# Kernel tuning notes

Hardware: AMD Instinct MI355X
Metric: run time of the kernel (lower is better)

Reference implementation:

```python
import jax, jax.numpy as jnp
import numpy as np

C = 256
CQ = max(1, C // 8)  # 32


def setup_inputs() -> dict:
    key = jax.random.key(0)
    ks = jax.random.split(key, 8)
    B, D, H, W = 4, 16, 16, 16
    x = jax.random.normal(ks[0], (B, C, D, H, W), dtype=jnp.float32)
    # 1x1 Conv3d == channel-wise linear; weights scaled ~1/sqrt(C) for stable softmax
    s = 0.05
    wq = jax.random.normal(ks[1], (CQ, C), dtype=jnp.float32) * s
    bq = jax.random.normal(ks[2], (CQ,), dtype=jnp.float32) * s
    wk = jax.random.normal(ks[3], (CQ, C), dtype=jnp.float32) * s
    bk = jax.random.normal(ks[4], (CQ,), dtype=jnp.float32) * s
    wv = jax.random.normal(ks[5], (C, C), dtype=jnp.float32) * s
    bv = jax.random.normal(ks[6], (C,), dtype=jnp.float32) * s
    gamma = jax.random.normal(ks[7], (1,), dtype=jnp.float32)
    return {"x": x, "wq": wq, "bq": bq, "wk": wk, "bk": bk,
            "wv": wv, "bv": bv, "gamma": gamma}


def reference(x, wq, bq, wk, bk, wv, bv, gamma):
    B, Cc, D, H, W = x.shape
    N = D * H * W
    xf = x.reshape(B, Cc, N)                                   # [B,C,N]
    # 1x1 conv projections (channel contractions)
    q = jnp.einsum('qc,bcn->bnq', wq, xf) + bq                 # [B,N,Cq]
    k = jnp.einsum('qc,bcn->bqn', wk, xf) + bk[None, :, None]  # [B,Cq,N]
    v = jnp.einsum('oc,bcn->bon', wv, xf) + bv[None, :, None]  # [B,C,N]
    att = jax.nn.softmax(jnp.einsum('bnq,bqm->bnm', q, k), axis=-1)  # [B,N,N]
    out = jnp.einsum('bom,bnm->bon', v, att)                   # [B,C,N]
    out = gamma[0] * out + xf
    return out.reshape(B, Cc, D, H, W)
```

## Files before the change

kernel.cpp:

```cpp
#include <hip/hip_runtime.h>
#include <stdint.h>

typedef unsigned short u16;
typedef unsigned int u32;
typedef short s16x8 __attribute__((ext_vector_type(8)));
typedef float f32x4 __attribute__((ext_vector_type(4)));
typedef float f32x16 __attribute__((ext_vector_type(16)));

#define LOG2E 1.44269504088896340736f
#define FIXMAX 40.0f

__device__ __forceinline__ u16 f2bf(float f) {
    union { float f; u32 i; } c; c.f = f;
    u32 u = c.i + 0x7FFFu + ((c.i >> 16) & 1u);
    return (u16)(u >> 16);
}
__device__ __forceinline__ float fast_exp2(float x) {
#if __has_builtin(__builtin_amdgcn_exp2f)
    return __builtin_amdgcn_exp2f(x);
#else
    return exp2f(x);
#endif
}
__device__ __forceinline__ u32 cvtpk_bf16(float lo, float hi) {
    u32 r;
    asm("v_cvt_pk_bf16_f32 %0, %1, %2" : "=v"(r) : "v"(lo), "v"(hi));
    return r;
}
__device__ __forceinline__ void swap32(u32 a, u32 b, u32& x, u32& y, int half) {
#if __has_builtin(__builtin_amdgcn_permlane32_swap)
    auto r = __builtin_amdgcn_permlane32_swap(a, b, false, false);
    x = r[0]; y = r[1];
#else
    u32 ax = (u32)__shfl_xor((int)a, 32, 64);
    u32 bx = (u32)__shfl_xor((int)b, 32, 64);
    x = half ? bx : a;
    y = half ? b : ax;
#endif
}


__global__ __launch_bounds__(256) void convert_w(
    const float* __restrict__ wq, const float* __restrict__ wk,
    const float* __restrict__ wv, u16* __restrict__ wsb)
{
    int i = blockIdx.x * 256 + threadIdx.x;
    float v;
    if (i < 65536)      v = wv[i];
    else if (i < 73728) v = wq[i - 65536];
    else                v = wk[i - 73728];
    wsb[i] = f2bf(v);
}

__global__ __launch_bounds__(256, 2) void proj_kernel(
    const float* __restrict__ x,
    const u16* __restrict__ wq_bf, const float* __restrict__ bq,
    const u16* __restrict__ wk_bf, const float* __restrict__ bk,
    const u16* __restrict__ wv_bf, const float* __restrict__ bv,
    u16* __restrict__ q_ws, u16* __restrict__ k_ws, u16* __restrict__ v_ws)
{
    __shared__ u16 XT[32 * 264];
    const int t  = threadIdx.x;
    const int b  = blockIdx.x >> 7;
    const int n0 = (blockIdx.x & 127) << 5;

    {
        const int c2 = t & 127;
        const int nh = (t >> 7) << 4;
        size_t base0 = (size_t)(b * 256 + 2 * c2) * 4096 + n0 + nh;
        float4 R0[4], R1[4];
        #pragma unroll
        for (int g = 0; g < 4; ++g) {
            R0[g] = *(const float4*)(x + base0 + 4 * g);
            R1[g] = *(const float4*)(x + base0 + 4096 + 4 * g);
        }
        u32* lds32 = (u32*)XT;
        #pragma unroll
        for (int g = 0; g < 4; ++g) {
            const float* p0 = (const float*)&R0[g];
            const float* p1 = (const float*)&R1[g];
            #pragma unroll
            for (int e = 0; e < 4; ++e) {
                int nl = nh + g * 4 + e;
                lds32[nl * 132 + c2] = (u32)f2bf(p0[e]) | ((u32)f2bf(p1[e]) << 16);
            }
        }
    }
    __syncthreads();

    const int wave = t >> 6, lane = t & 63, quad = lane >> 4, l15 = lane & 15;
    const int orow = wave * 64;

    f32x4 accV[4][2];
    f32x4 accQK[2];
    #pragma unroll
    for (int i = 0; i < 4; ++i) { accV[i][0] = (f32x4)0.0f; accV[i][1] = (f32x4)0.0f; }
    accQK[0] = (f32x4)0.0f; accQK[1] = (f32x4)0.0f;

    const int qsel = wave >> 1;
    const u16* wsel = qsel ? wk_bf : wq_bf;
    const int qc = ((wave & 1) << 4) + l15;

    #pragma unroll
    for (int co = 0; co < 8; ++co) {
        int cb = co * 32 + quad * 8;
        s16x8 X0 = *(const s16x8*)(XT + l15 * 264 + cb);
        s16x8 X1 = *(const s16x8*)(XT + (16 + l15) * 264 + cb);
        s16x8 WV[4];
        #pragma unroll
        for (int rt = 0; rt < 4; ++rt)
            WV[rt] = *(const s16x8*)(wv_bf + (size_t)(orow + rt * 16 + l15) * 256 + cb);
        s16x8 WQK = *(const s16x8*)(wsel + (size_t)qc * 256 + cb);

        #pragma unroll
        for (int rt = 0; rt < 4; ++rt) {
            accV[rt][0] = __builtin_amdgcn_mfma_f32_16x16x32_bf16(WV[rt], X0, accV[rt][0], 0, 0, 0);
            accV[rt][1] = __builtin_amdgcn_mfma_f32_16x16x32_bf16(WV[rt], X1, accV[rt][1], 0, 0, 0);
        }
        accQK[0] = __builtin_amdgcn_mfma_f32_16x16x32_bf16(X0, WQK, accQK[0], 0, 0, 0);
        accQK[1] = __builtin_amdgcn_mfma_f32_16x16x32_bf16(X1, WQK, accQK[1], 0, 0, 0);
    }

    {
        const int mh = (l15 >> 3) & 1;
        const int j  = l15 & 7;
        #pragma unroll
        for (int rt = 0; rt < 4; ++rt) {
            int ob = orow + rt * 16 + quad * 4;
            float bvf[4];
            #pragma unroll
            for (int r = 0; r < 4; ++r) bvf[r] = bv[ob + r];
            #pragma unroll
            for (int ct = 0; ct < 2; ++ct) {
                int kt = ((n0 + ct * 16) >> 4);
                #pragma unroll
                for (int r = 0; r < 4; ++r) {
                    int o = ob + r;
                    size_t addr = ((((size_t)(b * 256 + kt) * 8) + (o >> 5)) << 9)
                                + (size_t)((mh << 5) + (o & 31)) * 8 + j;
                    v_ws[addr] = f2bf(accV[rt][ct][r] + bvf[r]);
                }
            }
        }
    }
    if (qsel == 0) {
        float bias = bq[qc];
        #pragma unroll
        for (int r = 0; r < 2; ++r)
            #pragma unroll
            for (int reg = 0; reg < 4; ++reg) {
                int n = n0 + r * 16 + quad * 4 + reg;
                q_ws[(size_t)(b * 4096 + n) * 32 + qc] = f2bf((accQK[r][reg] + bias) * LOG2E);
            }
    } else {
        float bias = bk[qc];
        const int ckt = qc >> 4, ch2 = (qc >> 3) & 1, cj = qc & 7;
        #pragma unroll
        for (int r = 0; r < 2; ++r)
            #pragma unroll
            for (int reg = 0; reg < 4; ++reg) {
                int m = n0 + r * 16 + quad * 4 + reg;
                size_t addr = ((((size_t)(b * 128 + (m >> 5)) * 2) + ckt) << 9)
                            + (size_t)((ch2 << 5) + (m & 31)) * 8 + cj;
                k_ws[addr] = f2bf(accQK[r][reg] + bias);
            }
    }
}

__global__ __launch_bounds__(512, 2) void attn_kernel(
    const u16* __restrict__ q_ws, const u16* __restrict__ k_ws, const u16* __restrict__ v_ws,
    const float* __restrict__ x, const float* __restrict__ gamma_p, float* __restrict__ out)
{
    __shared__ float Ored[256 * 64];
    __shared__ float l_sh[4][2][64];

    const int t = threadIdx.x;
    const int wave = t >> 6, lane = t & 63;
    const int og = wave >> 2;
    const int ms = wave & 3;
    const int half = lane >> 5, n31 = lane & 31;

    const int bid = blockIdx.x;
    const int xcd = bid & 7;
    const int b   = xcd >> 1;
    const int nt  = ((xcd & 1) << 5) | (bid >> 3);
    const int n0  = nt << 6;

    const u16* qrow0 = q_ws + ((size_t)(b * 4096 + n0 + n31) << 5) + half * 8;
    const s16x8 QA0 = *(const s16x8*)(qrow0);
    const s16x8 QA1 = *(const s16x8*)(qrow0 + 16);
    const s16x8 QB0 = *(const s16x8*)(qrow0 + 1024);
    const s16x8 QB1 = *(const s16x8*)(qrow0 + 1024 + 16);

    const u16* kfb = k_ws + (((size_t)b * 256) << 9);
    const u16* vfb = v_ws + ((size_t)b << 20);

    f32x16 accO[4][2];
    #pragma unroll
    for (int ot = 0; ot < 4; ++ot) { accO[ot][0] = (f32x16)0.0f; accO[ot][1] = (f32x16)0.0f; }
    float l0_acc = 0.0f, l1_acc = 0.0f;

    for (int ch = 0; ch < 32; ++ch) {
        const int mt  = (ms << 5) + ch;
        const int ktb = mt << 1;

        const u16* kp = kfb + ((size_t)mt << 10) + lane * 8;
        s16x8 KF0 = *(const s16x8*)(kp);
        s16x8 KF1 = *(const s16x8*)(kp + 512);

        const u16* vp = vfb + (((size_t)(ktb * 8 + og * 4)) << 9) + lane * 8;
        s16x8 V0[4], V1[4];
        #pragma unroll
        for (int ot = 0; ot < 4; ++ot) {
            V0[ot] = *(const s16x8*)(vp + ot * 512);
            V1[ot] = *(const s16x8*)(vp + 4096 + ot * 512);
        }

        f32x16 st0 = (f32x16)0.0f, st1 = (f32x16)0.0f;
        st0 = __builtin_amdgcn_mfma_f32_32x32x16_bf16(KF0, QA0, st0, 0, 0, 0);
        st0 = __builtin_amdgcn_mfma_f32_32x32x16_bf16(KF1, QA1, st0, 0, 0, 0);
        st1 = __builtin_amdgcn_mfma_f32_32x32x16_bf16(KF0, QB0, st1, 0, 0, 0);
        st1 = __builtin_amdgcn_mfma_f32_32x32x16_bf16(KF1, QB1, st1, 0, 0, 0);

        float p0[16], p1[16];
        #pragma unroll
        for (int r = 0; r < 16; ++r) p0[r] = fast_exp2(st0[r] - FIXMAX);
        #pragma unroll
        for (int r = 0; r < 16; ++r) p1[r] = fast_exp2(st1[r] - FIXMAX);
        if (og == 0) {
            float a0 = (p0[0] + p0[1]) + (p0[2] + p0[3]);
            float a1 = (p0[4] + p0[5]) + (p0[6] + p0[7]);
            float a2 = (p0[8] + p0[9]) + (p0[10] + p0[11]);
            float a3 = (p0[12] + p0[13]) + (p0[14] + p0[15]);
            l0_acc += (a0 + a1) + (a2 + a3);
            float b0 = (p1[0] + p1[1]) + (p1[2] + p1[3]);
            float b1 = (p1[4] + p1[5]) + (p1[6] + p1[7]);
            float b2 = (p1[8] + p1[9]) + (p1[10] + p1[11]);
            float b3 = (p1[12] + p1[13]) + (p1[14] + p1[15]);
            l1_acc += (b0 + b1) + (b2 + b3);
        }

        union { u32 w[4]; s16x8 v; } P0B0, P0B1, P1B0, P1B1;
        {
            u32 A0 = cvtpk_bf16(p0[0],  p0[1]),  A1 = cvtpk_bf16(p0[2],  p0[3]);
            u32 B0 = cvtpk_bf16(p0[4],  p0[5]),  B1 = cvtpk_bf16(p0[6],  p0[7]);
            u32 C0 = cvtpk_bf16(p0[8],  p0[9]),  C1 = cvtpk_bf16(p0[10], p0[11]);
            u32 D0 = cvtpk_bf16(p0[12], p0[13]), D1 = cvtpk_bf16(p0[14], p0[15]);
            u32 w0, w1, w2, w3, y0, y1, y2, y3;
            swap32(A0, B0, w0, w2, half);
            swap32(A1, B1, w1, w3, half);
            swap32(C0, D0, y0, y2, half);
            swap32(C1, D1, y1, y3, half);
            P0B0.w[0] = w0; P0B0.w[1] = w1; P0B0.w[2] = w2; P0B0.w[3] = w3;
            P0B1.w[0] = y0; P0B1.w[1] = y1; P0B1.w[2] = y2; P0B1.w[3] = y3;
        }
        {
            u32 A0 = cvtpk_bf16(p1[0],  p1[1]),  A1 = cvtpk_bf16(p1[2],  p1[3]);
            u32 B0 = cvtpk_bf16(p1[4],  p1[5]),  B1 = cvtpk_bf16(p1[6],  p1[7]);
            u32 C0 = cvtpk_bf16(p1[8],  p1[9]),  C1 = cvtpk_bf16(p1[10], p1[11]);
            u32 D0 = cvtpk_bf16(p1[12], p1[13]), D1 = cvtpk_bf16(p1[14], p1[15]);
            u32 w0, w1, w2, w3, y0, y1, y2, y3;
            swap32(A0, B0, w0, w2, half);
            swap32(A1, B1, w1, w3, half);
            swap32(C0, D0, y0, y2, half);
            swap32(C1, D1, y1, y3, half);
            P1B0.w[0] = w0; P1B0.w[1] = w1; P1B0.w[2] = w2; P1B0.w[3] = w3;
            P1B1.w[0] = y0; P1B1.w[1] = y1; P1B1.w[2] = y2; P1B1.w[3] = y3;
        }

        #pragma unroll
        for (int ot = 0; ot < 4; ++ot) {
            accO[ot][0] = __builtin_amdgcn_mfma_f32_32x32x16_bf16(V0[ot], P0B0.v, accO[ot][0], 0, 0, 0);
            accO[ot][0] = __builtin_amdgcn_mfma_f32_32x32x16_bf16(V1[ot], P0B1.v, accO[ot][0], 0, 0, 0);
            accO[ot][1] = __builtin_amdgcn_mfma_f32_32x32x16_bf16(V0[ot], P1B0.v, accO[ot][1], 0, 0, 0);
            accO[ot][1] = __builtin_amdgcn_mfma_f32_32x32x16_bf16(V1[ot], P1B1.v, accO[ot][1], 0, 0, 0);
        }
    }

    if (og == 0) {
        l_sh[ms][half][n31]      = l0_acc;
        l_sh[ms][half][32 + n31] = l1_acc;
    }
    if (ms == 0) {
        #pragma unroll
        for (int ot = 0; ot < 4; ++ot)
            #pragma unroll
            for (int nhh = 0; nhh < 2; ++nhh)
                #pragma unroll
                for (int r = 0; r < 16; ++r) {
                    const int o = (og << 7) + (ot << 5) + (r & 3) + ((r >> 2) << 3) + (half << 2);
                    Ored[(o << 6) + (nhh << 5) + n31] = accO[ot][nhh][r];
                }
    }
    __syncthreads();
    #pragma unroll
    for (int s = 1; s < 4; ++s) {
        if (ms == s) {
            #pragma unroll
            for (int ot = 0; ot < 4; ++ot)
                #pragma unroll
                for (int nhh = 0; nhh < 2; ++nhh)
                    #pragma unroll
                    for (int r = 0; r < 16; ++r) {
                        const int o = (og << 7) + (ot << 5) + (r & 3) + ((r >> 2) << 3) + (half << 2);
                        Ored[(o << 6) + (nhh << 5) + n31] += accO[ot][nhh][r];
                    }
        }
        __syncthreads();
    }

    const float gamma = gamma_p[0];
    const int nn = t & 63;
    const int oo = t >> 6;
    float lt = 0.0f;
    #pragma unroll
    for (int s = 0; s < 4; ++s) lt += l_sh[s][0][nn] + l_sh[s][1][nn];
    const float rinv = gamma / lt;
    const int n = n0 + nn;
    #pragma unroll
    for (int i = 0; i < 32; ++i) {
        const int o = oo + (i << 3);
        const size_t idx = ((size_t)(b * 256 + o) << 12) + n;
        out[idx] = Ored[(o << 6) + nn] * rinv + x[idx];
    }
}

extern "C" void kernel_launch(void* const* d_in, const int* in_sizes, int n_in,
                              void* d_out, int out_size, void* d_ws, size_t ws_size,
                              hipStream_t stream) {
    const float* x  = (const float*)d_in[0];
    const float* wq = (const float*)d_in[1];
    const float* bq = (const float*)d_in[2];
    const float* wk = (const float*)d_in[3];
    const float* bk = (const float*)d_in[4];
    const float* wv = (const float*)d_in[5];
    const float* bv = (const float*)d_in[6];
    const float* gm = (const float*)d_in[7];

    u16* wsb   = (u16*)d_ws;
    u16* wv_bf = wsb;
    u16* wq_bf = wsb + 65536;
    u16* wk_bf = wsb + 73728;
    u16* q_ws  = wsb + 81920;
    u16* k_ws  = q_ws + 4 * 4096 * 32;
    u16* v_ws  = k_ws + 4 * 4096 * 32;

    convert_w<<<320, 256, 0, stream>>>(wq, wk, wv, wsb);
    proj_kernel<<<512, 256, 0, stream>>>(x, wq_bf, bq, wk_bf, bk, wv_bf, bv, q_ws, k_ws, v_ws);
    attn_kernel<<<256, 512, 0, stream>>>(q_ws, k_ws, v_ws, x, gm, (float*)d_out);
}
```

Baseline: 145.9 us.

## Fuse weight bf16 conversion into projection kernel and prefetch K fragments

Removes the separate convert_w launch. The projection kernel now reads fp32 weights and converts them to bf16 in registers with packed cvt instructions, which saves a launch and a workspace round trip. In exchange, each block reads twice as many weight bytes and does redundant conversions. The attention loop also software-prefetches the next K fragment after the QK MFMAs, so that load latency overlaps the softmax and PV work at some register cost.

```diff
diff --git a/kernel.cpp b/kernel.cpp
--- a/kernel.cpp
+++ b/kernel.cpp
@@ -26,6 +26,16 @@
     u32 r;
     asm("v_cvt_pk_bf16_f32 %0, %1, %2" : "=v"(r) : "v"(lo), "v"(hi));
     return r;
+}
+__device__ __forceinline__ s16x8 cvt8(const float* p) {
+    float4 a = *(const float4*)(p);
+    float4 b = *(const float4*)(p + 4);
+    union { u32 w[4]; s16x8 v; } r;
+    r.w[0] = cvtpk_bf16(a.x, a.y);
+    r.w[1] = cvtpk_bf16(a.z, a.w);
+    r.w[2] = cvtpk_bf16(b.x, b.y);
+    r.w[3] = cvtpk_bf16(b.z, b.w);
+    return r.v;
 }
 __device__ __forceinline__ void swap32(u32 a, u32 b, u32& x, u32& y, int half) {
 #if __has_builtin(__builtin_amdgcn_permlane32_swap)
@@ -40,23 +50,11 @@
 }
 
 
-__global__ __launch_bounds__(256) void convert_w(
-    const float* __restrict__ wq, const float* __restrict__ wk,
-    const float* __restrict__ wv, u16* __restrict__ wsb)
-{
-    int i = blockIdx.x * 256 + threadIdx.x;
-    float v;
-    if (i < 65536)      v = wv[i];
-    else if (i < 73728) v = wq[i - 65536];
-    else                v = wk[i - 73728];
-    wsb[i] = f2bf(v);
-}
-
 __global__ __launch_bounds__(256, 2) void proj_kernel(
     const float* __restrict__ x,
-    const u16* __restrict__ wq_bf, const float* __restrict__ bq,
-    const u16* __restrict__ wk_bf, const float* __restrict__ bk,
-    const u16* __restrict__ wv_bf, const float* __restrict__ bv,
+    const float* __restrict__ wq, const float* __restrict__ bq,
+    const float* __restrict__ wk, const float* __restrict__ bk,
+    const float* __restrict__ wv, const float* __restrict__ bv,
     u16* __restrict__ q_ws, u16* __restrict__ k_ws, u16* __restrict__ v_ws)
 {
     __shared__ u16 XT[32 * 264];
@@ -98,7 +96,7 @@
     accQK[0] = (f32x4)0.0f; accQK[1] = (f32x4)0.0f;
 
     const int qsel = wave >> 1;
-    const u16* wsel = qsel ? wk_bf : wq_bf;
+    const float* wsel = qsel ? wk : wq;
     const int qc = ((wave & 1) << 4) + l15;
 
     #pragma unroll
@@ -109,8 +107,8 @@
         s16x8 WV[4];
         #pragma unroll
         for (int rt = 0; rt < 4; ++rt)
-            WV[rt] = *(const s16x8*)(wv_bf + (size_t)(orow + rt * 16 + l15) * 256 + cb);
-        s16x8 WQK = *(const s16x8*)(wsel + (size_t)qc * 256 + cb);
+            WV[rt] = cvt8(wv + (size_t)(orow + rt * 16 + l15) * 256 + cb);
+        s16x8 WQK = cvt8(wsel + (size_t)qc * 256 + cb);
 
         #pragma unroll
         for (int rt = 0; rt < 4; ++rt) {
@@ -200,13 +198,16 @@
     for (int ot = 0; ot < 4; ++ot) { accO[ot][0] = (f32x16)0.0f; accO[ot][1] = (f32x16)0.0f; }
     float l0_acc = 0.0f, l1_acc = 0.0f;
 
+    {
+        const u16* kp0 = kfb + (((size_t)(ms << 5)) << 10) + lane * 8;
+    }
+    const u16* kp0 = kfb + (((size_t)(ms << 5)) << 10) + lane * 8;
+    s16x8 KF0 = *(const s16x8*)(kp0);
+    s16x8 KF1 = *(const s16x8*)(kp0 + 512);
+
     for (int ch = 0; ch < 32; ++ch) {
         const int mt  = (ms << 5) + ch;
         const int ktb = mt << 1;
-
-        const u16* kp = kfb + ((size_t)mt << 10) + lane * 8;
-        s16x8 KF0 = *(const s16x8*)(kp);
-        s16x8 KF1 = *(const s16x8*)(kp + 512);
 
         const u16* vp = vfb + (((size_t)(ktb * 8 + og * 4)) << 9) + lane * 8;
         s16x8 V0[4], V1[4];
@@ -221,6 +222,13 @@
         st0 = __builtin_amdgcn_mfma_f32_32x32x16_bf16(KF1, QA1, st0, 0, 0, 0);
         st1 = __builtin_amdgcn_mfma_f32_32x32x16_bf16(KF0, QB0, st1, 0, 0, 0);
         st1 = __builtin_amdgcn_mfma_f32_32x32x16_bf16(KF1, QB1, st1, 0, 0, 0);
+
+        {
+            const int mtn = (ch < 31) ? mt + 1 : mt;
+            const u16* kpn = kfb + ((size_t)mtn << 10) + lane * 8;
+            KF0 = *(const s16x8*)(kpn);
+            KF1 = *(const s16x8*)(kpn + 512);
+        }
 
         float p0[16], p1[16];
         #pragma unroll
@@ -337,15 +345,10 @@
     const float* bv = (const float*)d_in[6];
     const float* gm = (const float*)d_in[7];
 
-    u16* wsb   = (u16*)d_ws;
-    u16* wv_bf = wsb;
-    u16* wq_bf = wsb + 65536;
-    u16* wk_bf = wsb + 73728;
-    u16* q_ws  = wsb + 81920;
-    u16* k_ws  = q_ws + 4 * 4096 * 32;
-    u16* v_ws  = k_ws + 4 * 4096 * 32;
-
-    convert_w<<<320, 256, 0, stream>>>(wq, wk, wv, wsb);
-    proj_kernel<<<512, 256, 0, stream>>>(x, wq_bf, bq, wk_bf, bk, wv_bf, bv, q_ws, k_ws, v_ws);
+    u16* q_ws = (u16*)d_ws;
+    u16* k_ws = q_ws + 4 * 4096 * 32;
+    u16* v_ws = k_ws + 4 * 4096 * 32;
+
+    proj_kernel<<<512, 256, 0, stream>>>(x, wq, bq, wk, bk, wv, bv, q_ws, k_ws, v_ws);
     attn_kernel<<<256, 512, 0, stream>>>(q_ws, k_ws, v_ws, x, gm, (float*)d_out);
 }
```

Measured after the change: 153.7 us. 1.05x slower.

## Software-pipeline attention loop: overlap next QK^T/softmax with current PV MFMAs

Applied to the files above, without the earlier changes.

Restructures the attention chunk loop so the S=KQ MFMAs and exp/bf16 packing for chunk i+1 are issued alongside the PV MFMAs for chunk i, with K fragments prefetched two chunks ahead. A prologue and epilogue handle the first score tile and the last PV update. The aim is to hide the exp/convert/permlane latency and the dependent MFMA chain behind independent matrix work. In exchange it carries an extra set of packed P registers, which raises register pressure and could lower occupancy under launch_bounds(256,2).

```diff
diff --git a/kernel.cpp b/kernel.cpp
--- a/kernel.cpp
+++ b/kernel.cpp
@@ -37,6 +37,33 @@
     x = half ? bx : a;
     y = half ? b : ax;
 #endif
+}
+
+union PBu { u32 w[4]; s16x8 v; };
+
+__device__ __forceinline__ void sm_half(const f32x16& st, PBu& PB0, PBu& PB1,
+                                        float& l_acc, bool doL, int half) {
+    float p[16];
+    #pragma unroll
+    for (int r = 0; r < 16; ++r) p[r] = fast_exp2(st[r] - FIXMAX);
+    if (doL) {
+        float t0 = (p[0] + p[1]) + (p[2] + p[3]);
+        float t1 = (p[4] + p[5]) + (p[6] + p[7]);
+        float t2 = (p[8] + p[9]) + (p[10] + p[11]);
+        float t3 = (p[12] + p[13]) + (p[14] + p[15]);
+        l_acc += (t0 + t1) + (t2 + t3);
+    }
+    u32 A0 = cvtpk_bf16(p[0],  p[1]),  A1 = cvtpk_bf16(p[2],  p[3]);
+    u32 B0 = cvtpk_bf16(p[4],  p[5]),  B1 = cvtpk_bf16(p[6],  p[7]);
+    u32 C0 = cvtpk_bf16(p[8],  p[9]),  C1 = cvtpk_bf16(p[10], p[11]);
+    u32 D0 = cvtpk_bf16(p[12], p[13]), D1 = cvtpk_bf16(p[14], p[15]);
+    u32 w0, w1, w2, w3, y0, y1, y2, y3;
+    swap32(A0, B0, w0, w2, half);
+    swap32(A1, B1, w1, w3, half);
+    swap32(C0, D0, y0, y2, half);
+    swap32(C1, D1, y1, y3, half);
+    PB0.w[0] = w0; PB0.w[1] = w1; PB0.w[2] = w2; PB0.w[3] = w3;
+    PB1.w[0] = y0; PB1.w[1] = y1; PB1.w[2] = y2; PB1.w[3] = y3;
 }
 
 
@@ -199,81 +226,82 @@
     #pragma unroll
     for (int ot = 0; ot < 4; ++ot) { accO[ot][0] = (f32x16)0.0f; accO[ot][1] = (f32x16)0.0f; }
     float l0_acc = 0.0f, l1_acc = 0.0f;
-
-    for (int ch = 0; ch < 32; ++ch) {
-        const int mt  = (ms << 5) + ch;
-        const int ktb = mt << 1;
-
-        const u16* kp = kfb + ((size_t)mt << 10) + lane * 8;
-        s16x8 KF0 = *(const s16x8*)(kp);
-        s16x8 KF1 = *(const s16x8*)(kp + 512);
-
-        const u16* vp = vfb + (((size_t)(ktb * 8 + og * 4)) << 9) + lane * 8;
-        s16x8 V0[4], V1[4];
-        #pragma unroll
-        for (int ot = 0; ot < 4; ++ot) {
-            V0[ot] = *(const s16x8*)(vp + ot * 512);
-            V1[ot] = *(const s16x8*)(vp + 4096 + ot * 512);
-        }
-
+    const bool doL = (og == 0);
+
+    const int mtb = ms << 5;
+
+    s16x8 KF0, KF1;
+    {
+        const u16* kp = kfb + ((size_t)mtb << 10) + lane * 8;
+        KF0 = *(const s16x8*)(kp);
+        KF1 = *(const s16x8*)(kp + 512);
+    }
+    PBu pA0, pA1, pB0, pB1;
+    {
         f32x16 st0 = (f32x16)0.0f, st1 = (f32x16)0.0f;
         st0 = __builtin_amdgcn_mfma_f32_32x32x16_bf16(KF0, QA0, st0, 0, 0, 0);
         st0 = __builtin_amdgcn_mfma_f32_32x32x16_bf16(KF1, QA1, st0, 0, 0, 0);
         st1 = __builtin_amdgcn_mfma_f32_32x32x16_bf16(KF0, QB0, st1, 0, 0, 0);
         st1 = __builtin_amdgcn_mfma_f32_32x32x16_bf16(KF1, QB1, st1, 0, 0, 0);
-
-        float p0[16], p1[16];
-        #pragma unroll
-        for (int r = 0; r < 16; ++r) p0[r] = fast_exp2(st0[r] - FIXMAX);
-        #pragma unroll
-        for (int r = 0; r < 16; ++r) p1[r] = fast_exp2(st1[r] - FIXMAX);
-        if (og == 0) {
-            float a0 = (p0[0] + p0[1]) + (p0[2] + p0[3]);
-            float a1 = (p0[4] + p0[5]) + (p0[6] + p0[7]);
-            float a2 = (p0[8] + p0[9]) + (p0[10] + p0[11]);
-            float a3 = (p0[12] + p0[13]) + (p0[14] + p0[15]);
-            l0_acc += (a0 + a1) + (a2 + a3);
-            float b0 = (p1[0] + p1[1]) + (p1[2] + p1[3]);
-            float b1 = (p1[4] + p1[5]) + (p1[6] + p1[7]);
-            float b2 = (p1[8] + p1[9]) + (p1[10] + p1[11]);
-            float b3 = (p1[12] + p1[13]) + (p1[14] + p1[15]);
-            l1_acc += (b0 + b1) + (b2 + b3);
-        }
-
-        union { u32 w[4]; s16x8 v; } P0B0, P0B1, P1B0, P1B1;
-        {
-            u32 A0 = cvtpk_bf16(p0[0],  p0[1]),  A1 = cvtpk_bf16(p0[2],  p0[3]);
-            u32 B0 = cvtpk_bf16(p0[4],  p0[5]),  B1 = cvtpk_bf16(p0[6],  p0[7]);
-            u32 C0 = cvtpk_bf16(p0[8],  p0[9]),  C1 = cvtpk_bf16(p0[10], p0[11]);
-            u32 D0 = cvtpk_bf16(p0[12], p0[13]), D1 = cvtpk_bf16(p0[14], p0[15]);
-            u32 w0, w1, w2, w3, y0, y1, y2, y3;
-            swap32(A0, B0, w0, w2, half);
-            swap32(A1, B1, w1, w3, half);
-            swap32(C0, D0, y0, y2, half);
-            swap32(C1, D1, y1, y3, half);
-            P0B0.w[0] = w0; P0B0.w[1] = w1; P0B0.w[2] = w2; P0B0.w[3] = w3;
-            P0B1.w[0] = y0; P0B1.w[1] = y1; P0B1.w[2] = y2; P0B1.w[3] = y3;
-        }
-        {
-            u32 A0 = cvtpk_bf16(p1[0],  p1[1]),  A1 = cvtpk_bf16(p1[2],  p1[3]);
-            u32 B0 = cvtpk_bf16(p1[4],  p1[5]),  B1 = cvtpk_bf16(p1[6],  p1[7]);
-            u32 C0 = cvtpk_bf16(p1[8],  p1[9]),  C1 = cvtpk_bf16(p1[10], p1[11]);
-            u32 D0 = cvtpk_bf16(p1[12], p1[13]), D1 = cvtpk_bf16(p1[14], p1[15]);
-            u32 w0, w1, w2, w3, y0, y1, y2, y3;
-            swap32(A0, B0, w0, w2, half);
-            swap32(A1, B1, w1, w3, half);
-            swap32(C0, D0, y0, y2, half);
-            swap32(C1, D1, y1, y3, half);
-            P1B0.w[0] = w0; P1B0.w[1] = w1; P1B0.w[2] = w2; P1B0.w[3] = w3;
-            P1B1.w[0] = y0; P1B1.w[1] = y1; P1B1.w[2] = y2; P1B1.w[3] = y3;
-        }
-
+        const u16* kp = kfb + ((size_t)(mtb + 1) << 10) + lane * 8;
+        KF0 = *(const s16x8*)(kp);
+        KF1 = *(const s16x8*)(kp + 512);
+        sm_half(st0, pA0, pA1, l0_acc, doL, half);
+        sm_half(st1, pB0, pB1, l1_acc, doL, half);
+    }
+
+    for (int i = 0; i < 31; ++i) {
+        const int ktbPV = (mtb + i) << 1;
+        const u16* vp = vfb + (((size_t)(ktbPV * 8 + og * 4)) << 9) + lane * 8;
+        s16x8 V0[4], V1[4];
         #pragma unroll
         for (int ot = 0; ot < 4; ++ot) {
-            accO[ot][0] = __builtin_amdgcn_mfma_f32_32x32x16_bf16(V0[ot], P0B0.v, accO[ot][0], 0, 0, 0);
-            accO[ot][0] = __builtin_amdgcn_mfma_f32_32x32x16_bf16(V1[ot], P0B1.v, accO[ot][0], 0, 0, 0);
-            accO[ot][1] = __builtin_amdgcn_mfma_f32_32x32x16_bf16(V0[ot], P1B0.v, accO[ot][1], 0, 0, 0);
-            accO[ot][1] = __builtin_amdgcn_mfma_f32_32x32x16_bf16(V1[ot], P1B1.v, accO[ot][1], 0, 0, 0);
+            V0[ot] = *(const s16x8*)(vp + ot * 512);
+            V1[ot] = *(const s16x8*)(vp + 4096 + ot * 512);
+        }
+
+        f32x16 st0 = (f32x16)0.0f, st1 = (f32x16)0.0f;
+        st0 = __builtin_amdgcn_mfma_f32_32x32x16_bf16(KF0, QA0, st0, 0, 0, 0);
+        st0 = __builtin_amdgcn_mfma_f32_32x32x16_bf16(KF1, QA1, st0, 0, 0, 0);
+        st1 = __builtin_amdgcn_mfma_f32_32x32x16_bf16(KF0, QB0, st1, 0, 0, 0);
+        st1 = __builtin_amdgcn_mfma_f32_32x32x16_bf16(KF1, QB1, st1, 0, 0, 0);
+
+        if (i < 30) {
+            const u16* kp = kfb + ((size_t)(mtb + i + 2) << 10) + lane * 8;
+            KF0 = *(const s16x8*)(kp);
+            KF1 = *(const s16x8*)(kp + 512);
+        }
+
+        PBu nA0, nA1, nB0, nB1;
+        sm_half(st0, nA0, nA1, l0_acc, doL, half);
+        sm_half(st1, nB0, nB1, l1_acc, doL, half);
+
+        #pragma unroll
+        for (int ot = 0; ot < 4; ++ot) {
+            accO[ot][0] = __builtin_amdgcn_mfma_f32_32x32x16_bf16(V0[ot], pA0.v, accO[ot][0], 0, 0, 0);
+            accO[ot][0] = __builtin_amdgcn_mfma_f32_32x32x16_bf16(V1[ot], pA1.v, accO[ot][0], 0, 0, 0);
+            accO[ot][1] = __builtin_amdgcn_mfma_f32_32x32x16_bf16(V0[ot], pB0.v, accO[ot][1], 0, 0, 0);
+            accO[ot][1] = __builtin_amdgcn_mfma_f32_32x32x16_bf16(V1[ot], pB1.v, accO[ot][1], 0, 0, 0);
+        }
+
+        pA0 = nA0; pA1 = nA1; pB0 = nB0; pB1 = nB1;
+    }
+
+    {
+        const int ktbPV = (mtb + 31) << 1;
+        const u16* vp = vfb + (((size_t)(ktbPV * 8 + og * 4)) << 9) + lane * 8;
+        s16x8 V0[4], V1[4];
+        #pragma unroll
+        for (int ot = 0; ot < 4; ++ot) {
+            V0[ot] = *(const s16x8*)(vp + ot * 512);
+            V1[ot] = *(const s16x8*)(vp + 4096 + ot * 512);
+        }
+        #pragma unroll
+        for (int ot = 0; ot < 4; ++ot) {
+            accO[ot][0] = __builtin_amdgcn_mfma_f32_32x32x16_bf16(V0[ot], pA0.v, accO[ot][0], 0, 0, 0);
+            accO[ot][0] = __builtin_amdgcn_mfma_f32_32x32x16_bf16(V1[ot], pA1.v, accO[ot][0], 0, 0, 0);
+            accO[ot][1] = __builtin_amdgcn_mfma_f32_32x32x16_bf16(V0[ot], pB0.v, accO[ot][1], 0, 0, 0);
+            accO[ot][1] = __builtin_amdgcn_mfma_f32_32x32x16_bf16(V1[ot], pB1.v, accO[ot][1], 0, 0, 0);
         }
     }
 
```

New measurement: 149.1 us. +2.2%, slower.
